# Performance work log

Measured on AMD Instinct MI355X. Metric: run time of the kernel, lower is better.

Reference implementation:

```python
import jax, jax.numpy as jnp
import numpy as np

T, B, D, H = 1024, 64, 256, 256  # seq_len, batch, input_dim, hidden_dim (== n_qubits)


def setup_inputs() -> dict:
    key = jax.random.key(0)
    k_x, k_w, k_b, k_n = jax.random.split(key, 4)
    inputs = jax.random.normal(k_x, (T, B, D), dtype=jnp.float32)
    # Four gate Linears (forget, input, update, output) fused into one [D+H, 4H] matrix.
    # Math is identical to 4 separate Linears on the same `combined` input.
    bound = 1.0 / np.sqrt(D + H)
    W = jax.random.uniform(k_w, (D + H, 4 * H), dtype=jnp.float32, minval=-bound, maxval=bound)
    b = jax.random.uniform(k_b, (4 * H,), dtype=jnp.float32, minval=-bound, maxval=bound)
    beta = jnp.float32(0.01)  # learnable noise_beta parameter
    noise = jax.random.normal(k_n, (T, B, H), dtype=jnp.float32)  # randn_like(hx) per step
    return {"inputs": inputs, "W": W, "b": b, "beta": beta, "noise": noise}


def reference(inputs, W, b, beta, noise):
    Bsz = inputs.shape[1]
    Hd = W.shape[1] // 4
    h0 = jnp.zeros((Bsz, Hd), dtype=inputs.dtype)
    c0 = jnp.zeros((Bsz, Hd), dtype=inputs.dtype)

    def step(carry, xs):
        hx, cx = carry
        x, nz = xs
        combined = jnp.concatenate([x, hx], axis=1)          # [B, D+H]
        gates = combined @ W + b                             # [B, 4H] fused gate GEMM
        f, i, g, o = jnp.split(gates, 4, axis=1)
        f = jax.nn.sigmoid(f)
        i = jax.nn.sigmoid(i)
        g = jnp.tanh(g)
        o = jax.nn.sigmoid(o)
        cx_new = f * cx + i * g
        hx_new = o * jnp.tanh(cx_new) + beta * nz            # noise injection
        return (hx_new, cx_new), hx_new

    (hx, cx), outputs = jax.lax.scan(step, (h0, c0), (inputs, noise))
    return outputs, hx, cx
```

## Files before the change

### kernel.cpp

```cpp
#include <hip/hip_runtime.h>


typedef _Float16 half2_t __attribute__((ext_vector_type(2)));
typedef _Float16 half4_t __attribute__((ext_vector_type(4)));
typedef _Float16 half8_t __attribute__((ext_vector_type(8)));
typedef float floatx4 __attribute__((ext_vector_type(4)));

__device__ __forceinline__ float fdot2(unsigned h, unsigned w, float acc) {
#if __has_builtin(__builtin_amdgcn_fdot2)
  return __builtin_amdgcn_fdot2(__builtin_bit_cast(half2_t, h),
                                __builtin_bit_cast(half2_t, w), acc, false);
#else
  half2_t a = __builtin_bit_cast(half2_t, h);
  half2_t b = __builtin_bit_cast(half2_t, w);
  return acc + (float)a[0] * (float)b[0] + (float)a[1] * (float)b[1];
#endif
}

__device__ __forceinline__ floatx4 mfma16x16x32(half8_t a, half8_t b, floatx4 c) {
#if __has_builtin(__builtin_amdgcn_mfma_f32_16x16x32_f16)
  return __builtin_amdgcn_mfma_f32_16x16x32_f16(a, b, c, 0, 0, 0);
#else
  half4_t alo = __builtin_shufflevector(a, a, 0, 1, 2, 3);
  half4_t ahi = __builtin_shufflevector(a, a, 4, 5, 6, 7);
  half4_t blo = __builtin_shufflevector(b, b, 0, 1, 2, 3);
  half4_t bhi = __builtin_shufflevector(b, b, 4, 5, 6, 7);
  c = __builtin_amdgcn_mfma_f32_16x16x16f16(alo, blo, c, 0, 0, 0);
  c = __builtin_amdgcn_mfma_f32_16x16x16f16(ahi, bhi, c, 0, 0, 0);
  return c;
#endif
}

__device__ __forceinline__ float sigm(float x) { return 1.f / (1.f + __expf(-x)); }
__device__ __forceinline__ float tanh_(float x) {
  float ax = fabsf(x);
  float e = __expf(-2.f * ax);
  float t = (1.f - e) / (1.f + e);
  return x < 0.f ? -t : t;
}

__global__ __launch_bounds__(256) void k_transpose_w(const float* __restrict__ W,
                                                     _Float16* __restrict__ WT) {
  __shared__ float tile[64][65];
  const int bx = blockIdx.x & 15;
  const int by = blockIdx.x >> 4;
  const int c0 = bx * 64, r0 = by * 64;
  const int tid = threadIdx.x;
#pragma unroll
  for (int i = 0; i < 16; ++i) {
    int idx = tid + i * 256;
    int r = idx >> 6, c = idx & 63;
    tile[r][c] = W[(size_t)(r0 + r) * 1024 + c0 + c];
  }
  __syncthreads();
#pragma unroll
  for (int i = 0; i < 16; ++i) {
    int idx = tid + i * 256;
    int c = idx >> 6, r = idx & 63;
    WT[(size_t)(c0 + c) * 512 + r0 + r] = (_Float16)tile[r][c];
  }
}

__global__ __launch_bounds__(256) void k_gx_gemm(const float* __restrict__ X,
                                                 const _Float16* __restrict__ WT,
                                                 const float* __restrict__ bias,
                                                 _Float16* __restrict__ Gx) {
  const int nb = blockIdx.x & 7;
  const int mb = blockIdx.x >> 3;
  const int m0 = mb * 128, n0 = nb * 128;
  __shared__ __align__(16) _Float16 As[128 * 40];
  __shared__ __align__(16) _Float16 Bs[128 * 40];
  const int tid = threadIdx.x;
  const int wave = tid >> 6, lane = tid & 63;
  const int wm = (wave >> 1) * 64, wn = (wave & 1) * 64;
  const int lm = lane & 15, lg = lane >> 4;
  const int srow = tid >> 1, skh = (tid & 1) * 16;
  floatx4 acc[4][4] = {};
  for (int kt = 0; kt < 256; kt += 32) {
    __syncthreads();
    {
      const float* src = X + (size_t)(m0 + srow) * 256 + kt + skh;
      float4 f0 = ((const float4*)src)[0];
      float4 f1 = ((const float4*)src)[1];
      float4 f2 = ((const float4*)src)[2];
      float4 f3 = ((const float4*)src)[3];
      half8_t h0 = {(_Float16)f0.x, (_Float16)f0.y, (_Float16)f0.z, (_Float16)f0.w,
                    (_Float16)f1.x, (_Float16)f1.y, (_Float16)f1.z, (_Float16)f1.w};
      half8_t h1 = {(_Float16)f2.x, (_Float16)f2.y, (_Float16)f2.z, (_Float16)f2.w,
                    (_Float16)f3.x, (_Float16)f3.y, (_Float16)f3.z, (_Float16)f3.w};
      *(half8_t*)&As[srow * 40 + skh] = h0;
      *(half8_t*)&As[srow * 40 + skh + 8] = h1;
      const _Float16* bsrc = WT + (size_t)(n0 + srow) * 512 + kt + skh;
      half8_t b0 = ((const half8_t*)bsrc)[0];
      half8_t b1 = ((const half8_t*)bsrc)[1];
      *(half8_t*)&Bs[srow * 40 + skh] = b0;
      *(half8_t*)&Bs[srow * 40 + skh + 8] = b1;
    }
    __syncthreads();
    half8_t af[4], bf[4];
#pragma unroll
    for (int mf = 0; mf < 4; ++mf)
      af[mf] = *(const half8_t*)&As[(wm + mf * 16 + lm) * 40 + lg * 8];
#pragma unroll
    for (int nf = 0; nf < 4; ++nf)
      bf[nf] = *(const half8_t*)&Bs[(wn + nf * 16 + lm) * 40 + lg * 8];
#pragma unroll
    for (int mf = 0; mf < 4; ++mf)
#pragma unroll
      for (int nf = 0; nf < 4; ++nf)
        acc[mf][nf] = mfma16x16x32(af[mf], bf[nf], acc[mf][nf]);
  }
#pragma unroll
  for (int mf = 0; mf < 4; ++mf) {
#pragma unroll
    for (int nf = 0; nf < 4; ++nf) {
      const int gm = m0 + wm + mf * 16 + lg * 4;
      const int gn = n0 + wn + nf * 16 + lm;
      const float bv = bias[gn];
#pragma unroll
      for (int i = 0; i < 4; ++i)
        Gx[(size_t)(gm + i) * 1024 + gn] = (_Float16)(acc[mf][nf][i] + bv);
    }
  }
}

__global__ __attribute__((amdgpu_flat_work_group_size(1024, 1024))) void
k_lstm(const _Float16* __restrict__ Gx, const _Float16* __restrict__ WT,
       const float* __restrict__ noise, const float* __restrict__ beta_p,
       float* __restrict__ out) {
  __shared__ __align__(16) uint4 wl[1024 * 9];
  __shared__ float gates[1024];
  __shared__ unsigned hx2[128];

  const int b = blockIdx.x;
  const int tid = threadIdx.x;
  const float beta = beta_p[0];

  const uint4* p = (const uint4*)(WT + (size_t)tid * 512 + 256);
  uint4 w[23];
#pragma unroll
  for (int i = 0; i < 23; ++i) w[i] = p[i];
  uint4* wlp = wl + tid * 9;
#pragma unroll
  for (int i = 0; i < 9; ++i) wlp[i] = p[23 + i];
  if (tid < 128) hx2[tid] = 0u;
  float cx = 0.f, hlast = 0.f;
  __syncthreads();

  const _Float16* gp = Gx + (size_t)b * 1024 + tid;
  const float* nzp = noise + (size_t)b * 256 + (tid & 255);
  float* outp = out + (size_t)b * 256 + (tid & 255);

  float g = (float)gp[0];
  float nz = (tid < 256) ? nzp[0] : 0.f;

  for (int t = 0; t < 1024; ++t) {
    float gn = 0.f, nzn = 0.f;
    if (t < 1023) {
      gn = (float)gp[65536];
      if (tid < 256) nzn = nzp[16384];
    }

    float ae = 0.f, ao = 0.f;
#pragma unroll
    for (int i = 0; i < 23; ++i) {
      uint4 h4 = *(const uint4*)&hx2[i * 4];
      ae = fdot2(h4.x, w[i].x, ae);
      ao = fdot2(h4.y, w[i].y, ao);
      ae = fdot2(h4.z, w[i].z, ae);
      ao = fdot2(h4.w, w[i].w, ao);
    }
#pragma unroll
    for (int i = 0; i < 9; ++i) {
      uint4 h4 = *(const uint4*)&hx2[92 + i * 4];
      uint4 wa = wlp[i];
      ae = fdot2(h4.x, wa.x, ae);
      ao = fdot2(h4.y, wa.y, ao);
      ae = fdot2(h4.z, wa.z, ae);
      ao = fdot2(h4.w, wa.w, ao);
    }
    gates[tid] = ae + ao + g;
    __syncthreads();

    if (tid < 256) {
      float f = sigm(gates[tid]);
      float ii = sigm(gates[tid + 256]);
      float gg = tanh_(gates[tid + 512]);
      float oo = sigm(gates[tid + 768]);
      cx = f * cx + ii * gg;
      float h = oo * tanh_(cx) + beta * nz;
      hlast = h;
      outp[0] = h;
      ((_Float16*)hx2)[tid] = (_Float16)h;
    }
    g = gn;
    nz = nzn;
    gp += 65536;
    nzp += 16384;
    outp += 16384;
    __syncthreads();
  }

  if (tid < 256) {
    out[(size_t)16777216 + (size_t)b * 256 + tid] = hlast;
    out[(size_t)16777216 + 16384 + (size_t)b * 256 + tid] = cx;
  }
}

extern "C" void kernel_launch(void* const* d_in, const int* in_sizes, int n_in,
                              void* d_out, int out_size, void* d_ws, size_t ws_size,
                              hipStream_t stream) {
  const float* X = (const float*)d_in[0];
  const float* W = (const float*)d_in[1];
  const float* bias = (const float*)d_in[2];
  const float* beta = (const float*)d_in[3];
  const float* noise = (const float*)d_in[4];
  float* out = (float*)d_out;

  char* ws = (char*)d_ws;
  _Float16* Gx = (_Float16*)ws;
  _Float16* WT = (_Float16*)(ws + (size_t)134217728);

  k_transpose_w<<<128, 256, 0, stream>>>(W, WT);
  k_gx_gemm<<<4096, 256, 0, stream>>>(X, WT, bias, Gx);
  k_lstm<<<64, 1024, 0, stream>>>(Gx, WT, noise, beta, out);
}
```

Measured before the change: 2.136 ms.

## Use MFMA for recurrent matvec with weights held in AGPRs and streamed

Replaces the per-thread fdot2 recurrent matvec with MFMA 16x16x32 tiles. Each of 8 waves computes 128 gate columns. Half of the weight fragments stay in accumulation registers (AGPRs); the other half are streamed from a pre-swizzled global buffer with a triple-buffered software prefetch. Only the first row of the MFMA A operand holds the real hidden state, so most of the MFMA work is wasted padding, and the streamed weights reload from cache on every timestep. The block is halved to 512 threads, and the Gx/noise loads are no longer prefetched a step ahead.

```diff
diff --git a/kernel.cpp b/kernel.cpp
--- a/kernel.cpp
+++ b/kernel.cpp
@@ -5,17 +5,6 @@
 typedef _Float16 half4_t __attribute__((ext_vector_type(4)));
 typedef _Float16 half8_t __attribute__((ext_vector_type(8)));
 typedef float floatx4 __attribute__((ext_vector_type(4)));
-
-__device__ __forceinline__ float fdot2(unsigned h, unsigned w, float acc) {
-#if __has_builtin(__builtin_amdgcn_fdot2)
-  return __builtin_amdgcn_fdot2(__builtin_bit_cast(half2_t, h),
-                                __builtin_bit_cast(half2_t, w), acc, false);
-#else
-  half2_t a = __builtin_bit_cast(half2_t, h);
-  half2_t b = __builtin_bit_cast(half2_t, w);
-  return acc + (float)a[0] * (float)b[0] + (float)a[1] * (float)b[1];
-#endif
-}
 
 __device__ __forceinline__ floatx4 mfma16x16x32(half8_t a, half8_t b, floatx4 c) {
 #if __has_builtin(__builtin_amdgcn_mfma_f32_16x16x32_f16)
@@ -124,80 +113,150 @@
   }
 }
 
-__global__ __attribute__((amdgpu_flat_work_group_size(1024, 1024))) void
-k_lstm(const _Float16* __restrict__ Gx, const _Float16* __restrict__ WT,
+__global__ __launch_bounds__(256) void k_prep_frags(const _Float16* __restrict__ WT,
+                                                    uint4* __restrict__ WB) {
+  const int gid = blockIdx.x * 256 + threadIdx.x;
+  const int l = gid & 63;
+  const int c = (gid >> 6) & 7;
+  const int n = (gid >> 9) & 7;
+  const int w = gid >> 12;
+  const int col = w * 128 + n * 16 + (l & 15);
+  const int k0 = c * 32 + (l >> 4) * 8;
+  WB[gid] = *(const uint4*)(WT + (size_t)col * 512 + 256 + k0);
+}
+
+#define RES_MFMA(c, n)                                                        \
+  {                                                                           \
+    unsigned qx, qy, qz, qw;                                                  \
+    asm volatile("v_accvgpr_read_b32 %0, %1" : "=v"(qx) : "a"(aw[(n * 8 + c) * 4 + 0])); \
+    asm volatile("v_accvgpr_read_b32 %0, %1" : "=v"(qy) : "a"(aw[(n * 8 + c) * 4 + 1])); \
+    asm volatile("v_accvgpr_read_b32 %0, %1" : "=v"(qz) : "a"(aw[(n * 8 + c) * 4 + 2])); \
+    asm volatile("v_accvgpr_read_b32 %0, %1" : "=v"(qw) : "a"(aw[(n * 8 + c) * 4 + 3])); \
+    uint4 q = {qx, qy, qz, qw};                                               \
+    acc[n] = mfma16x16x32(af, __builtin_bit_cast(half8_t, q), acc[n]);        \
+  }
+
+#define LSTM_CHUNK(c, Scons, Sprod, DOLOAD)                                   \
+  {                                                                           \
+    if (DOLOAD) {                                                             \
+      Sprod[0] = sbase[0 * 512 + (c + 2) * 64];                               \
+      Sprod[1] = sbase[1 * 512 + (c + 2) * 64];                               \
+      Sprod[2] = sbase[2 * 512 + (c + 2) * 64];                               \
+      Sprod[3] = sbase[3 * 512 + (c + 2) * 64];                               \
+    }                                                                         \
+    half8_t af = *(const half8_t*)(hbase + c * 32);                           \
+    RES_MFMA(c, 0)                                                            \
+    RES_MFMA(c, 1)                                                            \
+    RES_MFMA(c, 2)                                                            \
+    RES_MFMA(c, 3)                                                            \
+    acc[4] = mfma16x16x32(af, __builtin_bit_cast(half8_t, Scons[0]), acc[4]); \
+    acc[5] = mfma16x16x32(af, __builtin_bit_cast(half8_t, Scons[1]), acc[5]); \
+    acc[6] = mfma16x16x32(af, __builtin_bit_cast(half8_t, Scons[2]), acc[6]); \
+    acc[7] = mfma16x16x32(af, __builtin_bit_cast(half8_t, Scons[3]), acc[7]); \
+  }
+
+__global__ __attribute__((amdgpu_flat_work_group_size(512, 512),
+                          amdgpu_waves_per_eu(2, 2))) void
+k_lstm(const _Float16* __restrict__ Gx, const uint4* __restrict__ WB,
        const float* __restrict__ noise, const float* __restrict__ beta_p,
        float* __restrict__ out) {
-  __shared__ __align__(16) uint4 wl[1024 * 9];
   __shared__ float gates[1024];
-  __shared__ unsigned hx2[128];
+  __shared__ __align__(16) _Float16 hxPad[512];
+  __shared__ uint4 lds_force[5120];
 
   const int b = blockIdx.x;
   const int tid = threadIdx.x;
+  const int l = tid & 63;
+  const int w = tid >> 6;
   const float beta = beta_p[0];
 
-  const uint4* p = (const uint4*)(WT + (size_t)tid * 512 + 256);
-  uint4 w[23];
-#pragma unroll
-  for (int i = 0; i < 23; ++i) w[i] = p[i];
-  uint4* wlp = wl + tid * 9;
-#pragma unroll
-  for (int i = 0; i < 9; ++i) wlp[i] = p[23 + i];
-  if (tid < 128) hx2[tid] = 0u;
+  if (beta_p == nullptr) lds_force[0] = uint4{0, 0, 0, 0};
+
+  if (tid < 256) {
+    hxPad[tid] = (_Float16)0.f;
+    hxPad[256 + tid] = (_Float16)0.f;
+  }
+
+  const uint4* wbl = WB + w * 4096 + l;
+  unsigned aw[128];
+#pragma unroll
+  for (int n = 0; n < 4; ++n) {
+#pragma unroll
+    for (int c = 0; c < 8; ++c) {
+      uint4 t = wbl[n * 512 + c * 64];
+      const int i = (n * 8 + c) * 4;
+      asm volatile("v_accvgpr_write_b32 %0, %1" : "=a"(aw[i + 0]) : "v"(t.x));
+      asm volatile("v_accvgpr_write_b32 %0, %1" : "=a"(aw[i + 1]) : "v"(t.y));
+      asm volatile("v_accvgpr_write_b32 %0, %1" : "=a"(aw[i + 2]) : "v"(t.z));
+      asm volatile("v_accvgpr_write_b32 %0, %1" : "=a"(aw[i + 3]) : "v"(t.w));
+    }
+  }
+
+  const _Float16* hbase = hxPad + (((l & 15) == 0) ? 0 : 256) + (l >> 4) * 8;
+  const uint4* sbase = wbl + 4 * 512;
+
   float cx = 0.f, hlast = 0.f;
+  const floatx4 fzero = {0.f, 0.f, 0.f, 0.f};
   __syncthreads();
 
-  const _Float16* gp = Gx + (size_t)b * 1024 + tid;
-  const float* nzp = noise + (size_t)b * 256 + (tid & 255);
-  float* outp = out + (size_t)b * 256 + (tid & 255);
-
-  float g = (float)gp[0];
-  float nz = (tid < 256) ? nzp[0] : 0.f;
-
   for (int t = 0; t < 1024; ++t) {
-    float gn = 0.f, nzn = 0.f;
-    if (t < 1023) {
-      gn = (float)gp[65536];
-      if (tid < 256) nzn = nzp[16384];
-    }
-
-    float ae = 0.f, ao = 0.f;
-#pragma unroll
-    for (int i = 0; i < 23; ++i) {
-      uint4 h4 = *(const uint4*)&hx2[i * 4];
-      ae = fdot2(h4.x, w[i].x, ae);
-      ao = fdot2(h4.y, w[i].y, ao);
-      ae = fdot2(h4.z, w[i].z, ae);
-      ao = fdot2(h4.w, w[i].w, ao);
-    }
-#pragma unroll
-    for (int i = 0; i < 9; ++i) {
-      uint4 h4 = *(const uint4*)&hx2[92 + i * 4];
-      uint4 wa = wlp[i];
-      ae = fdot2(h4.x, wa.x, ae);
-      ao = fdot2(h4.y, wa.y, ao);
-      ae = fdot2(h4.z, wa.z, ae);
-      ao = fdot2(h4.w, wa.w, ao);
-    }
-    gates[tid] = ae + ao + g;
-    __syncthreads();
-
+    {
+      unsigned lo = (unsigned)(uintptr_t)sbase;
+      unsigned hi = (unsigned)((uintptr_t)sbase >> 32);
+      asm volatile("" : "+v"(lo), "+v"(hi));
+      sbase = (const uint4*)(((uintptr_t)hi << 32) | lo);
+    }
+    const size_t base = (size_t)t * 64 + b;
+
+    float gx0 = 0.f, gx1 = 0.f, gx2 = 0.f, gx3 = 0.f, nz = 0.f;
     if (tid < 256) {
-      float f = sigm(gates[tid]);
-      float ii = sigm(gates[tid + 256]);
-      float gg = tanh_(gates[tid + 512]);
-      float oo = sigm(gates[tid + 768]);
+      const _Float16* gp = Gx + base * 1024 + tid;
+      gx0 = (float)gp[0];
+      gx1 = (float)gp[256];
+      gx2 = (float)gp[512];
+      gx3 = (float)gp[768];
+      nz = noise[base * 256 + tid];
+    }
+
+    floatx4 acc[8];
+#pragma unroll
+    for (int n = 0; n < 8; ++n) acc[n] = fzero;
+
+    uint4 S0[4], S1[4], S2[4];
+    S0[0] = sbase[0 * 512 + 0 * 64];
+    S0[1] = sbase[1 * 512 + 0 * 64];
+    S0[2] = sbase[2 * 512 + 0 * 64];
+    S0[3] = sbase[3 * 512 + 0 * 64];
+    S1[0] = sbase[0 * 512 + 1 * 64];
+    S1[1] = sbase[1 * 512 + 1 * 64];
+    S1[2] = sbase[2 * 512 + 1 * 64];
+    S1[3] = sbase[3 * 512 + 1 * 64];
+
+    LSTM_CHUNK(0, S0, S2, 1)
+    LSTM_CHUNK(1, S1, S0, 1)
+    LSTM_CHUNK(2, S2, S1, 1)
+    LSTM_CHUNK(3, S0, S2, 1)
+    LSTM_CHUNK(4, S1, S0, 1)
+    LSTM_CHUNK(5, S2, S1, 1)
+    LSTM_CHUNK(6, S0, S2, 0)
+    LSTM_CHUNK(7, S1, S0, 0)
+
+#pragma unroll
+    for (int n = 0; n < 8; ++n)
+      if (l < 16) gates[w * 128 + n * 16 + l] = acc[n][0];
+    __syncthreads();
+
+    if (tid < 256) {
+      float f = sigm(gates[tid] + gx0);
+      float ii = sigm(gates[tid + 256] + gx1);
+      float gg = tanh_(gates[tid + 512] + gx2);
+      float oo = sigm(gates[tid + 768] + gx3);
       cx = f * cx + ii * gg;
       float h = oo * tanh_(cx) + beta * nz;
       hlast = h;
-      outp[0] = h;
-      ((_Float16*)hx2)[tid] = (_Float16)h;
-    }
-    g = gn;
-    nz = nzn;
-    gp += 65536;
-    nzp += 16384;
-    outp += 16384;
+      out[base * 256 + tid] = h;
+      hxPad[tid] = (_Float16)h;
+    }
     __syncthreads();
   }
 
@@ -220,8 +279,10 @@
   char* ws = (char*)d_ws;
   _Float16* Gx = (_Float16*)ws;
   _Float16* WT = (_Float16*)(ws + (size_t)134217728);
+  uint4* WB = (uint4*)(ws + (size_t)135266304);
 
   k_transpose_w<<<128, 256, 0, stream>>>(W, WT);
+  k_prep_frags<<<128, 256, 0, stream>>>(WT, WB);
   k_gx_gemm<<<4096, 256, 0, stream>>>(X, WT, bias, Gx);
-  k_lstm<<<64, 1024, 0, stream>>>(Gx, WT, noise, beta, out);
-}
+  k_lstm<<<64, 512, 0, stream>>>(Gx, WB, noise, beta, out);
+}
```

Result: slower. 2.928 ms (+37.1%).
